# Optimization experiments

Hardware: AMD Instinct MI355X
Metric: run time of the kernel (lower is better)

The kernel has to match this reference:

```python
import jax, jax.numpy as jnp
import numpy as np


def setup_inputs() -> dict:
    key = jax.random.key(0)
    k1, k2 = jax.random.split(key)
    x = jax.random.normal(k1, (32, 16, 256, 256), dtype=jnp.float32)
    weight = jax.random.normal(k2, (5, 5), dtype=jnp.float32)
    return {"input": x, "weight": weight}


def reference(input, weight):
    # Original: per-(n,m) FFT-based 'full' 2D convolution with a shared 5x5 kernel.
    # Full linear convolution == correlation with the flipped kernel and (p-1, q-1) padding.
    a, b, c, d = input.shape
    p, q = weight.shape
    x = input.reshape(a * b, 1, c, d)                 # fold (batch, channel) into batch; 1 feature channel
    w = weight[::-1, ::-1].reshape(1, 1, p, q)        # flip kernel: lax conv is cross-correlation
    out = jax.lax.conv_general_dilated(
        x, w,
        window_strides=(1, 1),
        padding=((p - 1, p - 1), (q - 1, q - 1)),     # 'full' convolution
        dimension_numbers=("NCHW", "OIHW", "NCHW"),
    )
    return out.reshape(a, b, c + p - 1, d + q - 1)
```

## Files before the change

kernel.cpp:

```cpp
#include <hip/hip_runtime.h>


#define IMG 256
#define OW  260
#define TXN 65
#define ROWS 10
#define WROWS 14
#define STRIPS 26
#define NIMG 512
#define NTHREADS (NIMG * STRIPS * TXN)

__global__ __launch_bounds__(256, 3) void conv_full_strip3(
    const float* __restrict__ in, const float* __restrict__ w,
    float* __restrict__ out)
{
    float wt[25];
#pragma unroll
    for (int i = 0; i < 25; ++i) wt[i] = w[i];

    int idx = blockIdx.x * 256 + threadIdx.x;
    int tx4 = idx % TXN;
    int t   = idx / TXN;
    int s   = t % STRIPS;
    int n   = t / STRIPS;
    int y0  = s * ROWS;
    int x0  = tx4 * 4;

    int xl = x0 - 4; if (xl < 0) xl = 0;
    int xh = x0;     if (xh > IMG - 4) xh = IMG - 4;
    const bool zL = (tx4 == 0);
    const bool zR = (tx4 == TXN - 1);

    const float* img = in + (size_t)n * IMG * IMG;

    float4 rawL[WROWS], rawH[WROWS];
#pragma unroll
    for (int r = 0; r < WROWS; ++r) {
        int yy = y0 + r - 4;
        int yc = yy < 0 ? 0 : (yy > IMG - 1 ? IMG - 1 : yy);
        const float* rb = img + yc * IMG;
        rawL[r] = *(const float4*)(rb + xl);
        rawH[r] = *(const float4*)(rb + xh);
    }

    float v[WROWS][8];
#pragma unroll
    for (int r = 0; r < WROWS; ++r) {
        int yy = y0 + r - 4;
        bool rv = (yy >= 0) & (yy < IMG);
        bool mL = rv & !zL;
        bool mR = rv & !zR;
        v[r][0] = mL ? rawL[r].x : 0.f;
        v[r][1] = mL ? rawL[r].y : 0.f;
        v[r][2] = mL ? rawL[r].z : 0.f;
        v[r][3] = mL ? rawL[r].w : 0.f;
        v[r][4] = mR ? rawH[r].x : 0.f;
        v[r][5] = mR ? rawH[r].y : 0.f;
        v[r][6] = mR ? rawH[r].z : 0.f;
        v[r][7] = mR ? rawH[r].w : 0.f;
    }

    float* outp = out + (((size_t)n * OW + y0) * TXN + tx4) * 4;
#pragma unroll
    for (int r = 0; r < ROWS; ++r) {
        float acc0 = 0.f, acc1 = 0.f, acc2 = 0.f, acc3 = 0.f;
#pragma unroll
        for (int a = 0; a < 5; ++a) {
            const float* vv = v[r + 4 - a];
#pragma unroll
            for (int b = 0; b < 5; ++b) {
                float wv = wt[a * 5 + b];
                acc0 = fmaf(vv[4 - b], wv, acc0);
                acc1 = fmaf(vv[5 - b], wv, acc1);
                acc2 = fmaf(vv[6 - b], wv, acc2);
                acc3 = fmaf(vv[7 - b], wv, acc3);
            }
        }
        *(float4*)(outp + (size_t)r * OW) = make_float4(acc0, acc1, acc2, acc3);
    }
}

extern "C" void kernel_launch(void* const* d_in, const int* in_sizes, int n_in,
                              void* d_out, int out_size, void* d_ws, size_t ws_size,
                              hipStream_t stream) {
    const float* in = (const float*)d_in[0];
    const float* w  = (const float*)d_in[1];
    float* out = (float*)d_out;

    int blocks = NTHREADS / 256;
    conv_full_strip3<<<blocks, 256, 0, stream>>>(in, w, out);
}
```

Baseline: 243.8 us.

## Stream input rows with rolling accumulators and smaller strips for higher occupancy

Cuts the per-thread strip from 10 to 4 output rows. Input rows are loaded in a software-pipelined stream three rows ahead, and each row is scattered into the rolling accumulators of the output rows it touches. This removes the large register window, so launch bounds can allow 8 waves per SIMD, and weight loads are made wave-uniform via readfirstlane. The trade-off is more redundant halo reads: 8 input rows per 4 output rows instead of 14 per 10.

```diff
diff --git a/kernel.cpp b/kernel.cpp
--- a/kernel.cpp
+++ b/kernel.cpp
@@ -4,19 +4,29 @@
 #define IMG 256
 #define OW  260
 #define TXN 65
-#define ROWS 10
-#define WROWS 14
-#define STRIPS 26
+#define ROWS 4
+#define IROWS 8
+#define STRIPS 65
 #define NIMG 512
 #define NTHREADS (NIMG * STRIPS * TXN)
 
-__global__ __launch_bounds__(256, 3) void conv_full_strip3(
+#define ISSUE(rr)                                                         \
+    {                                                                     \
+        int yy = y0 + (rr) - 4;                                           \
+        int yc = yy < 0 ? 0 : (yy > IMG - 1 ? IMG - 1 : yy);              \
+        const float* rb = img + yc * IMG;                                 \
+        rawL[rr] = *(const float4*)(rb + xl);                             \
+        rawH[rr] = *(const float4*)(rb + xh);                             \
+    }
+
+__global__ __launch_bounds__(256, 8) void conv_full_stream4(
     const float* __restrict__ in, const float* __restrict__ w,
     float* __restrict__ out)
 {
     float wt[25];
 #pragma unroll
-    for (int i = 0; i < 25; ++i) wt[i] = w[i];
+    for (int i = 0; i < 25; ++i)
+        wt[i] = __int_as_float(__builtin_amdgcn_readfirstlane(__float_as_int(w[i])));
 
     int idx = blockIdx.x * 256 + threadIdx.x;
     int tx4 = idx % TXN;
@@ -31,53 +41,56 @@
     const bool zL = (tx4 == 0);
     const bool zR = (tx4 == TXN - 1);
 
-    const float* img = in + (size_t)n * IMG * IMG;
+    const float* img = in + (size_t)n * (IMG * IMG);
 
-    float4 rawL[WROWS], rawH[WROWS];
+    float4 rawL[IROWS], rawH[IROWS];
+
+    ISSUE(0); ISSUE(1); ISSUE(2);
+
+    float acc[ROWS][4];
 #pragma unroll
-    for (int r = 0; r < WROWS; ++r) {
-        int yy = y0 + r - 4;
-        int yc = yy < 0 ? 0 : (yy > IMG - 1 ? IMG - 1 : yy);
-        const float* rb = img + yc * IMG;
-        rawL[r] = *(const float4*)(rb + xl);
-        rawH[r] = *(const float4*)(rb + xh);
-    }
+    for (int r = 0; r < ROWS; ++r)
+        acc[r][0] = acc[r][1] = acc[r][2] = acc[r][3] = 0.f;
 
-    float v[WROWS][8];
 #pragma unroll
-    for (int r = 0; r < WROWS; ++r) {
-        int yy = y0 + r - 4;
+    for (int rr = 0; rr < IROWS; ++rr) {
+        if (rr + 3 < IROWS) ISSUE(rr + 3);
+
+        int yy = y0 + rr - 4;
         bool rv = (yy >= 0) & (yy < IMG);
         bool mL = rv & !zL;
         bool mR = rv & !zR;
-        v[r][0] = mL ? rawL[r].x : 0.f;
-        v[r][1] = mL ? rawL[r].y : 0.f;
-        v[r][2] = mL ? rawL[r].z : 0.f;
-        v[r][3] = mL ? rawL[r].w : 0.f;
-        v[r][4] = mR ? rawH[r].x : 0.f;
-        v[r][5] = mR ? rawH[r].y : 0.f;
-        v[r][6] = mR ? rawH[r].z : 0.f;
-        v[r][7] = mR ? rawH[r].w : 0.f;
+        float v[8];
+        v[0] = mL ? rawL[rr].x : 0.f;
+        v[1] = mL ? rawL[rr].y : 0.f;
+        v[2] = mL ? rawL[rr].z : 0.f;
+        v[3] = mL ? rawL[rr].w : 0.f;
+        v[4] = mR ? rawH[rr].x : 0.f;
+        v[5] = mR ? rawH[rr].y : 0.f;
+        v[6] = mR ? rawH[rr].z : 0.f;
+        v[7] = mR ? rawH[rr].w : 0.f;
+
+#pragma unroll
+        for (int r = 0; r < ROWS; ++r) {
+            const int a = r - rr + 4;
+            if (a >= 0 && a <= 4) {
+#pragma unroll
+                for (int b = 0; b < 5; ++b) {
+                    float wv = wt[a * 5 + b];
+                    acc[r][0] = fmaf(v[4 - b], wv, acc[r][0]);
+                    acc[r][1] = fmaf(v[5 - b], wv, acc[r][1]);
+                    acc[r][2] = fmaf(v[6 - b], wv, acc[r][2]);
+                    acc[r][3] = fmaf(v[7 - b], wv, acc[r][3]);
+                }
+            }
+        }
     }
 
     float* outp = out + (((size_t)n * OW + y0) * TXN + tx4) * 4;
 #pragma unroll
-    for (int r = 0; r < ROWS; ++r) {
-        float acc0 = 0.f, acc1 = 0.f, acc2 = 0.f, acc3 = 0.f;
-#pragma unroll
-        for (int a = 0; a < 5; ++a) {
-            const float* vv = v[r + 4 - a];
-#pragma unroll
-            for (int b = 0; b < 5; ++b) {
-                float wv = wt[a * 5 + b];
-                acc0 = fmaf(vv[4 - b], wv, acc0);
-                acc1 = fmaf(vv[5 - b], wv, acc1);
-                acc2 = fmaf(vv[6 - b], wv, acc2);
-                acc3 = fmaf(vv[7 - b], wv, acc3);
-            }
-        }
-        *(float4*)(outp + (size_t)r * OW) = make_float4(acc0, acc1, acc2, acc3);
-    }
+    for (int r = 0; r < ROWS; ++r)
+        *(float4*)(outp + (size_t)r * OW) =
+            make_float4(acc[r][0], acc[r][1], acc[r][2], acc[r][3]);
 }
 
 extern "C" void kernel_launch(void* const* d_in, const int* in_sizes, int n_in,
@@ -88,5 +101,5 @@
     float* out = (float*)d_out;
 
     int blocks = NTHREADS / 256;
-    conv_full_strip3<<<blocks, 256, 0, stream>>>(in, w, out);
+    conv_full_stream4<<<blocks, 256, 0, stream>>>(in, w, out);
 }
```

After: 291.4 us. +19.5%, slower.
